# Performance work log

Measured on AMD Instinct MI355X. Metric: run time of the kernel, lower is better.

The kernel has to match this reference:

```python
import jax, jax.numpy as jnp
import numpy as np

HEADS = 8
EPS = 1e-5

def _layer_norm(x, gamma, beta):
    mu = jnp.mean(x, axis=-1, keepdims=True)
    var = jnp.var(x, axis=-1, keepdims=True)
    return (x - mu) * jax.lax.rsqrt(var + EPS) * gamma + beta

def setup_inputs() -> dict:
    key = jax.random.key(0)
    ks = jax.random.split(key, 12)
    B, N, D, H = 4, 2048, 512, 2048
    s = lambda d: 1.0 / np.sqrt(d)
    return {
        "x": jax.random.normal(ks[0], (B, N, D), jnp.float32),
        "w_qkv": jax.random.normal(ks[1], (D, 3 * D), jnp.float32) * s(D),
        "b_qkv": jnp.zeros((3 * D,), jnp.float32),
        "w_proj": jax.random.normal(ks[2], (D, D), jnp.float32) * s(D),
        "b_proj": jnp.zeros((D,), jnp.float32),
        "ln1_g": jnp.ones((D,), jnp.float32),
        "ln1_b": jnp.zeros((D,), jnp.float32),
        "w1": jax.random.normal(ks[3], (D, H), jnp.float32) * s(D),
        "b1": jnp.zeros((H,), jnp.float32),
        "w2": jax.random.normal(ks[4], (H, D), jnp.float32) * s(H),
        "b2": jnp.zeros((D,), jnp.float32),
        "ln2_g": jnp.ones((D,), jnp.float32),
        "ln2_b": jnp.zeros((D,), jnp.float32),
    }

def reference(x, w_qkv, b_qkv, w_proj, b_proj, ln1_g, ln1_b, w1, b1, w2, b2, ln2_g, ln2_b):
    B, N, D = x.shape
    hd = D // HEADS
    scaling = hd ** (-0.5)
    # fused QKV projection: [b, n, 3*D] -> u=3, h heads
    qkv = x @ w_qkv + b_qkv
    qkv = qkv.reshape(B, N, 3, HEADS, hd)            # 'b n (u h e)' with u outermost
    q, k, v = (qkv[:, :, 0], qkv[:, :, 1], qkv[:, :, 2])  # each [b, n, h, e]
    q = q.transpose(0, 2, 1, 3); k = k.transpose(0, 2, 1, 3); v = v.transpose(0, 2, 1, 3)
    sim = jnp.einsum('bhqe,bhke->bhqk', q, k)        # NO pre-softmax scaling
    sim = jax.nn.softmax(sim, axis=-1) * scaling     # scaling applied AFTER softmax
    att = jnp.einsum('bhqk,bhke->bhqe', sim, v)
    att = att.transpose(0, 2, 1, 3).reshape(B, N, D)
    att = att @ w_proj + b_proj
    x = _layer_norm(x + att, ln1_g, ln1_b)
    # MLP sublayer (exact GELU as in torch nn.GELU default)
    h = jax.nn.gelu(x @ w1 + b1, approximate=False) @ w2 + b2
    x = _layer_norm(x + h, ln2_g, ln2_b)
    return x
```

## Files before the change

### kernel.cpp

```cpp
#include <hip/hip_runtime.h>

#define HEADS 8
#define Bq 4
#define Nq 2048
#define Dq 512
#define Hq 2048

typedef __bf16 bf16;
typedef __bf16 bf16x8 __attribute__((ext_vector_type(8)));
typedef __bf16 bf16x4 __attribute__((ext_vector_type(4)));
typedef short short4v __attribute__((ext_vector_type(4)));
typedef float f32x4 __attribute__((ext_vector_type(4)));

__device__ __forceinline__ void gload16(const bf16* g, bf16* s) {
  __builtin_amdgcn_global_load_lds(
      (const __attribute__((address_space(1))) void*)g,
      (__attribute__((address_space(3))) void*)s, 16, 0, 0);
}

__device__ __forceinline__ float fexp2(float x) {
#if __has_builtin(__builtin_amdgcn_exp2f)
  return __builtin_amdgcn_exp2f(x);
#else
  return exp2f(x);
#endif
}

__device__ __forceinline__ float frcp(float x) {
#if __has_builtin(__builtin_amdgcn_rcpf)
  return __builtin_amdgcn_rcpf(x);
#else
  return 1.f / x;
#endif
}

__device__ __forceinline__ float fgelu(float v) {
  float u = 0.7978845608f * (v + 0.044715f * v * v * v);
  float e = fexp2(u * 2.885390082f);
  return v * e * frcp(e + 1.f);
}

#define VM_BARRIER(N)                                         \
  do {                                                        \
    asm volatile("s_waitcnt vmcnt(" #N ")" ::: "memory");     \
    __builtin_amdgcn_s_barrier();                             \
    asm volatile("" ::: "memory");                            \
  } while (0)
#define END_BARRIER()                                         \
  do {                                                        \
    asm volatile("" ::: "memory");                            \
    __builtin_amdgcn_s_barrier();                             \
    asm volatile("" ::: "memory");                            \
  } while (0)

__global__ __launch_bounds__(256) void k_cvt_bf16(const float* __restrict__ in,
                                                  bf16* __restrict__ out, int n) {
  int i = (blockIdx.x * 256 + threadIdx.x) * 4;
  if (i >= n) return;
  float4 v = *(const float4*)(in + i);
  union { bf16 h[4]; ushort4 u; } r;
  r.h[0] = (bf16)v.x; r.h[1] = (bf16)v.y; r.h[2] = (bf16)v.z; r.h[3] = (bf16)v.w;
  *(ushort4*)(out + i) = r.u;
}

__global__ __launch_bounds__(256) void k_wtrans(const float* __restrict__ w_qkv,
                                                const float* __restrict__ w_proj,
                                                const float* __restrict__ w1,
                                                const float* __restrict__ w2,
                                                bf16* __restrict__ wqkvT,
                                                bf16* __restrict__ wprojT,
                                                bf16* __restrict__ w1T,
                                                bf16* __restrict__ w2T) {
  __shared__ float t[32][33];
  const int bid = blockIdx.x;
  const float* src;
  bf16* dst;
  int K, N, n0, k0;
  if (bid < 768) {
    src = w_qkv; dst = wqkvT; K = 512; N = 1536;
    n0 = (bid % 48) * 32; k0 = (bid / 48) * 32;
  } else if (bid < 1024) {
    int i = bid - 768;
    src = w_proj; dst = wprojT; K = 512; N = 512;
    n0 = (i % 16) * 32; k0 = (i / 16) * 32;
  } else if (bid < 2048) {
    int i = bid - 1024;
    src = w1; dst = w1T; K = 512; N = 2048;
    n0 = (i % 64) * 32; k0 = (i / 64) * 32;
  } else {
    int i = bid - 2048;
    src = w2; dst = w2T; K = 2048; N = 512;
    n0 = (i % 16) * 32; k0 = (i / 16) * 32;
  }
  const int tx = threadIdx.x, ty = threadIdx.y;
#pragma unroll
  for (int j = 0; j < 32; j += 8)
    t[ty + j][tx] = src[(size_t)(k0 + ty + j) * N + n0 + tx];
  __syncthreads();
#pragma unroll
  for (int j = 0; j < 32; j += 8)
    dst[(size_t)(n0 + ty + j) * K + k0 + tx] = (bf16)t[tx][ty + j];
}

template <int BM, bool GELU, bool RESID, bool STORE_BF16>
__global__ __launch_bounds__(512, 4) void k_gemm(const bf16* __restrict__ A,
                                                 const bf16* __restrict__ BT,
                                                 const float* __restrict__ bias,
                                                 const float* __restrict__ resid,
                                                 void* __restrict__ Cout,
                                                 int M, int N, int K, int GX) {
  constexpr int MI = BM / 32;
  constexpr int AROUNDS = BM / 64;
  constexpr size_t MAIN = (size_t)2 * (BM + 128) * 64 * 2;
  constexpr size_t CST = (size_t)BM * 136 * (STORE_BF16 ? 2 : 4);
  constexpr size_t SMEM = MAIN > CST ? MAIN : CST;
  __shared__ __align__(16) char smem[SMEM];
  bf16* Asb = (bf16*)smem;
  bf16* Bsb = Asb + 2 * BM * 64;

  const int nwg = gridDim.x;
  const int id = blockIdx.x;
  const int swz = (id & 7) * (nwg >> 3) + (id >> 3);
  const int bx = swz % GX, by = swz / GX;
  const int m0 = by * BM, n0 = bx * 128;

  const int tid = threadIdx.x, lane = tid & 63, wid = tid >> 6;
  const int wr = wid >> 2, wc = wid & 3;
  const int r16 = lane & 15, g = lane >> 4;
  const int lrow = lane >> 3;
  const int sch = (lane & 7) ^ lrow;

  f32x4 acc[MI][2] = {};

  const int NT = K >> 6;
  auto stage = [&](int t, int buf) {
    const int k0 = t << 6;
#pragma unroll
    for (int i = 0; i < AROUNDS; i++) {
      int row = i * 64 + wid * 8 + lrow;
      gload16(A + (size_t)(m0 + row) * K + k0 + sch * 8,
              Asb + buf * BM * 64 + (i * 64 + wid * 8) * 64);
    }
#pragma unroll
    for (int i = 0; i < 2; i++) {
      int row = i * 64 + wid * 8 + lrow;
      gload16(BT + (size_t)(n0 + row) * K + k0 + sch * 8,
              Bsb + buf * 128 * 64 + (i * 64 + wid * 8) * 64);
    }
  };
  auto compute = [&](const bf16* Ab, const bf16* Bb) {
#pragma unroll
    for (int kk = 0; kk < 2; kk++) {
      bf16x8 af[MI], bfr[2];
#pragma unroll
      for (int mi = 0; mi < MI; mi++)
        af[mi] = *(const bf16x8*)(Ab + (wr * (BM / 2) + mi * 16 + r16) * 64 +
                                  (((kk * 4 + g) ^ (r16 & 7)) * 8));
#pragma unroll
      for (int ni = 0; ni < 2; ni++)
        bfr[ni] = *(const bf16x8*)(Bb + (wc * 32 + ni * 16 + r16) * 64 +
                                   (((kk * 4 + g) ^ (r16 & 7)) * 8));
#pragma unroll
      for (int mi = 0; mi < MI; mi++)
#pragma unroll
        for (int ni = 0; ni < 2; ni++)
          acc[mi][ni] = __builtin_amdgcn_mfma_f32_16x16x32_bf16(af[mi], bfr[ni],
                                                                acc[mi][ni], 0, 0, 0);
    }
  };

  stage(0, 0);
  __syncthreads();

  for (int t = 0; t < NT; t += 2) {
    if (t + 1 < NT) stage(t + 1, 1);
    compute(Asb, Bsb);
    __syncthreads();
    if (t + 2 < NT) stage(t + 2, 0);
    compute(Asb + BM * 64, Bsb + 128 * 64);
    __syncthreads();
  }

  float bv[2];
#pragma unroll
  for (int ni = 0; ni < 2; ni++) bv[ni] = bias[n0 + wc * 32 + ni * 16 + r16];

  if (STORE_BF16) {
    bf16* Cl = (bf16*)smem;
#pragma unroll
    for (int mi = 0; mi < MI; mi++)
#pragma unroll
      for (int ni = 0; ni < 2; ni++)
#pragma unroll
        for (int r = 0; r < 4; r++) {
          float v = acc[mi][ni][r] + bv[ni];
          if (GELU) v = fgelu(v);
          Cl[(wr * (BM / 2) + mi * 16 + 4 * g + r) * 136 + wc * 32 + ni * 16 + r16] =
              (bf16)v;
        }
    __syncthreads();
    constexpr int ROWS_PER = 512 * 8 / 128;
#pragma unroll
    for (int rr = 0; rr < BM / ROWS_PER; rr++) {
      int row = rr * ROWS_PER + (tid >> 4);
      int cc = (tid & 15) * 8;
      bf16x8 v = *(const bf16x8*)(Cl + row * 136 + cc);
      *(bf16x8*)((bf16*)Cout + (size_t)(m0 + row) * N + n0 + cc) = v;
    }
  } else {
    float* Cl = (float*)smem;
#pragma unroll
    for (int mi = 0; mi < MI; mi++)
#pragma unroll
      for (int ni = 0; ni < 2; ni++)
#pragma unroll
        for (int r = 0; r < 4; r++) {
          float v = acc[mi][ni][r] + bv[ni];
          if (GELU) v = fgelu(v);
          Cl[(wr * (BM / 2) + mi * 16 + 4 * g + r) * 136 + wc * 32 + ni * 16 + r16] = v;
        }
    __syncthreads();
    constexpr int ROWS_PER = 512 * 4 / 128;
#pragma unroll
    for (int rr = 0; rr < BM / ROWS_PER; rr++) {
      int row = rr * ROWS_PER + (tid >> 5);
      int cc = (tid & 31) * 4;
      f32x4 v = *(const f32x4*)(Cl + row * 136 + cc);
      if (RESID) {
        f32x4 rv = *(const f32x4*)(resid + (size_t)(m0 + row) * N + n0 + cc);
        v += rv;
      }
      *(f32x4*)((float*)Cout + (size_t)(m0 + row) * N + n0 + cc) = v;
    }
  }
}

__global__ __launch_bounds__(256) void k_vtrans(const bf16* __restrict__ qkv,
                                                bf16* __restrict__ vt) {
  __shared__ bf16 T[64 * 66];
  const int kvb = blockIdx.x, bh = blockIdx.y;
  const int b = bh >> 3, h = bh & 7;
  const int tid = threadIdx.x, lane = tid & 63, w = tid >> 6;
  const bf16* src = qkv + ((size_t)b * Nq + kvb * 64) * (3 * Dq) + 2 * Dq + h * 64;
#pragma unroll
  for (int i = 0; i < 2; i++) {
    int u = tid + i * 256;
    int r = u >> 3, ch = u & 7;
    *(int4*)(&T[r * 66 + ch * 8]) = *(const int4*)(src + (size_t)r * (3 * Dq) + ch * 8);
  }
  __syncthreads();
  bf16* dst = vt + (size_t)bh * 64 * Nq + kvb * 64 + lane;
#pragma unroll
  for (int it = 0; it < 16; it++) {
    int e = w * 16 + it;
    dst[(size_t)e * Nq] = T[lane * 66 + e];
  }
}

__global__ __launch_bounds__(256) void k_attn(const bf16* __restrict__ qkv,
                                              const bf16* __restrict__ vt,
                                              bf16* __restrict__ att) {
  __shared__ bf16 Ks[2][64 * 64];
  __shared__ bf16 Vs[2][64 * 64];
  const int qt = blockIdx.y, b = blockIdx.x >> 3, h = blockIdx.x & 7;
  const int tid = threadIdx.x, lane = tid & 63, wid = tid >> 6;
  const int r16 = lane & 15, g = lane >> 4;
  const size_t base = (size_t)b * Nq * (3 * Dq);
  const bf16* qp = qkv + base + h * 64;
  const bf16* kp = qkv + base + Dq + h * 64;
  const bf16* vtp = vt + (size_t)(b * HEADS + h) * 64 * Nq;
  const int q0 = qt * 64 + wid * 16;

  bf16x8 qf[2];
#pragma unroll
  for (int kk = 0; kk < 2; kk++) {
    bf16x8 q = *(const bf16x8*)(qp + (size_t)(q0 + r16) * (3 * Dq) + kk * 32 + g * 8);
#pragma unroll
    for (int j = 0; j < 8; j++) q[j] = (bf16)((float)q[j] * 1.44269504f);
    qf[kk] = q;
  }

  const int srow = lane >> 3;
  const int sch = (lane & 7) ^ srow;
  int fsrc[2];
#pragma unroll
  for (int i = 0; i < 2; i++) {
    int d = (wid * 2 + i) * 8 + srow;
    fsrc[i] = ((d >> 5) << 5) + 8 * ((d & 15) >> 2) + 4 * ((d >> 4) & 1) + (d & 3);
  }

  bf16x8 ones8;
#pragma unroll
  for (int j = 0; j < 8; j++) ones8[j] = (bf16)1.f;

  f32x4 o[4] = {};
  f32x4 ol = {};

#pragma unroll
  for (int i = 0; i < 2; i++) {
    int br = (wid * 2 + i) * 8;
    gload16(kp + (size_t)fsrc[i] * (3 * Dq) + sch * 8, &Ks[0][br * 64]);
    gload16(vtp + (size_t)(br + srow) * Nq + sch * 8, &Vs[0][br * 64]);
  }
  __syncthreads();

  const int NTILES = Nq / 64;
  auto tile = [&](int t, int c) {
    if (t + 1 < NTILES) {
      const int kv1 = (t + 1) * 64;
#pragma unroll
      for (int i = 0; i < 2; i++) {
        int br = (wid * 2 + i) * 8;
        gload16(kp + (size_t)(kv1 + fsrc[i]) * (3 * Dq) + sch * 8,
                &Ks[c ^ 1][br * 64]);
        gload16(vtp + (size_t)(br + srow) * Nq + kv1 + sch * 8, &Vs[c ^ 1][br * 64]);
      }
      VM_BARRIER(4);
    } else {
      VM_BARRIER(0);
    }

    f32x4 s[4] = {};
    __builtin_amdgcn_s_setprio(1);
#pragma unroll
    for (int kk = 0; kk < 2; kk++)
#pragma unroll
      for (int nt = 0; nt < 4; nt++) {
        const bf16x8 kf = *(const bf16x8*)(
            &Ks[c][(nt * 16 + r16) * 64 + (((4 * kk + g) ^ (r16 & 7)) * 8)]);
        s[nt] = __builtin_amdgcn_mfma_f32_16x16x32_bf16(kf, qf[kk], s[nt], 0, 0, 0);
      }
    __builtin_amdgcn_s_setprio(0);

#pragma unroll
    for (int nt = 0; nt < 4; nt++)
#pragma unroll
      for (int r = 0; r < 4; r++) s[nt][r] = fexp2(s[nt][r]);

    bf16x8 pb[2];
#pragma unroll
    for (int kk = 0; kk < 2; kk++) {
      bf16x8 t8;
#pragma unroll
      for (int r = 0; r < 4; r++) {
        t8[r] = (bf16)s[2 * kk][r];
        t8[4 + r] = (bf16)s[2 * kk + 1][r];
      }
      pb[kk] = t8;
    }

    __builtin_amdgcn_s_setprio(1);
    ol = __builtin_amdgcn_mfma_f32_16x16x32_bf16(ones8, pb[0], ol, 0, 0, 0);
    ol = __builtin_amdgcn_mfma_f32_16x16x32_bf16(ones8, pb[1], ol, 0, 0, 0);
#pragma unroll
    for (int kk = 0; kk < 2; kk++)
#pragma unroll
      for (int ot = 0; ot < 4; ot++) {
        const bf16x8 vf = *(const bf16x8*)(
            &Vs[c][(ot * 16 + r16) * 64 + (((kk * 4 + g) ^ (r16 & 7)) * 8)]);
        o[ot] = __builtin_amdgcn_mfma_f32_16x16x32_bf16(vf, pb[kk], o[ot], 0, 0, 0);
      }
    __builtin_amdgcn_s_setprio(0);
    END_BARRIER();
  };

  for (int t = 0; t < NTILES; t += 2) {
    tile(t, 0);
    tile(t + 1, 1);
  }

  asm volatile("s_nop 7\ns_nop 7");

  const float li = 0.125f / ol[0];
  const size_t rowoff = ((size_t)b * Nq + q0 + r16) * Dq + h * 64;
#pragma unroll
  for (int ot = 0; ot < 4; ot++) {
    union { bf16 h[4]; ushort4 u; } r4;
#pragma unroll
    for (int r = 0; r < 4; r++) r4.h[r] = (bf16)(o[ot][r] * li);
    *(ushort4*)(att + rowoff + ot * 16 + 4 * g) = r4.u;
  }
}

template <bool WB>
__global__ __launch_bounds__(256) void k_ln(const float* __restrict__ in,
                                            const float* __restrict__ gamma,
                                            const float* __restrict__ beta,
                                            float* __restrict__ outf,
                                            bf16* __restrict__ outb) {
  const int row = blockIdx.x * 4 + threadIdx.y;
  const int lane = threadIdx.x;
  const float* p = in + (size_t)row * Dq + lane * 8;
  float4 a = *(const float4*)p;
  float4 c = *(const float4*)(p + 4);
  float vals[8] = {a.x, a.y, a.z, a.w, c.x, c.y, c.z, c.w};
  float s = 0.f, q = 0.f;
#pragma unroll
  for (int j = 0; j < 8; j++) { s += vals[j]; q += vals[j] * vals[j]; }
#pragma unroll
  for (int off = 1; off < 64; off <<= 1) {
    s += __shfl_xor(s, off);
    q += __shfl_xor(q, off);
  }
  float mean = s * (1.f / Dq);
  float var = q * (1.f / Dq) - mean * mean;
  float rstd = rsqrtf(var + 1e-5f);
  float of[8];
#pragma unroll
  for (int j = 0; j < 8; j++) {
    int col = lane * 8 + j;
    of[j] = (vals[j] - mean) * rstd * gamma[col] + beta[col];
  }
  float4* op = (float4*)(outf + (size_t)row * Dq + lane * 8);
  op[0] = make_float4(of[0], of[1], of[2], of[3]);
  op[1] = make_float4(of[4], of[5], of[6], of[7]);
  if (WB) {
    union { bf16 h[8]; ushort4 u[2]; } rr;
#pragma unroll
    for (int j = 0; j < 8; j++) rr.h[j] = (bf16)of[j];
    ushort4* ob = (ushort4*)(outb + (size_t)row * Dq + lane * 8);
    ob[0] = rr.u[0];
    ob[1] = rr.u[1];
  }
}

extern "C" void kernel_launch(void* const* d_in, const int* in_sizes, int n_in,
                              void* d_out, int out_size, void* d_ws, size_t ws_size,
                              hipStream_t stream) {
  const float* x      = (const float*)d_in[0];
  const float* w_qkv  = (const float*)d_in[1];
  const float* b_qkv  = (const float*)d_in[2];
  const float* w_proj = (const float*)d_in[3];
  const float* b_proj = (const float*)d_in[4];
  const float* ln1_g  = (const float*)d_in[5];
  const float* ln1_b  = (const float*)d_in[6];
  const float* w1     = (const float*)d_in[7];
  const float* b1     = (const float*)d_in[8];
  const float* w2     = (const float*)d_in[9];
  const float* b2     = (const float*)d_in[10];
  const float* ln2_g  = (const float*)d_in[11];
  const float* ln2_b  = (const float*)d_in[12];
  float* out = (float*)d_out;

  const int M = Bq * Nq;

  char* p = (char*)d_ws;
  auto alloc = [&](size_t bytes) -> void* {
    char* r = p;
    p += (bytes + 255) & ~(size_t)255;
    return (void*)r;
  };
  bf16* xb     = (bf16*)alloc((size_t)M * Dq * 2);
  bf16* qkvb   = (bf16*)alloc((size_t)M * 3 * Dq * 2);
  bf16* wqkvT  = (bf16*)alloc((size_t)3 * Dq * Dq * 2);
  bf16* wprojT = (bf16*)alloc((size_t)Dq * Dq * 2);
  bf16* w1T    = (bf16*)alloc((size_t)Hq * Dq * 2);
  bf16* w2T    = (bf16*)alloc((size_t)Dq * Hq * 2);
  float* y1    = (float*)alloc((size_t)M * Dq * 4);
  float* x1f   = (float*)alloc((size_t)M * Dq * 4);
  bf16* x1b    = (bf16*)alloc((size_t)M * Dq * 2);
  bf16* hb     = (bf16*)alloc((size_t)M * Hq * 2);
  bf16* attb   = xb;
  bf16* vtb    = hb;

  dim3 tb(32, 8);
  k_cvt_bf16<<<(M * Dq / 4 + 255) / 256, 256, 0, stream>>>(x, xb, M * Dq);
  k_wtrans<<<3072, tb, 0, stream>>>(w_qkv, w_proj, w1, w2, wqkvT, wprojT, w1T, w2T);

  k_gemm<128, false, false, true><<<768, 512, 0, stream>>>(
      xb, wqkvT, b_qkv, nullptr, qkvb, M, 3 * Dq, Dq, 12);
  k_vtrans<<<dim3(Nq / 64, Bq * HEADS), 256, 0, stream>>>(qkvb, vtb);
  k_attn<<<dim3(Bq * HEADS, Nq / 64), 256, 0, stream>>>(qkvb, vtb, attb);
  k_gemm<64, false, true, false><<<512, 512, 0, stream>>>(
      attb, wprojT, b_proj, x, y1, M, Dq, Dq, 4);
  k_ln<true><<<M / 4, dim3(64, 4), 0, stream>>>(y1, ln1_g, ln1_b, x1f, x1b);
  k_gemm<128, true, false, true><<<1024, 512, 0, stream>>>(
      x1b, w1T, b1, nullptr, hb, M, Hq, Dq, 16);
  k_gemm<64, false, true, false><<<512, 512, 0, stream>>>(
      hb, w2T, b2, x1f, y1, M, Dq, Hq, 4);
  k_ln<false><<<M / 4, dim3(64, 4), 0, stream>>>(y1, ln2_g, ln2_b, out, nullptr);
}
```

Baseline: 161.4 us.

## Fuse V transpose into QKV GEMM epilogue and store residual sums in bf16

```diff
diff --git a/kernel.cpp b/kernel.cpp
--- a/kernel.cpp
+++ b/kernel.cpp
@@ -102,17 +102,18 @@
     dst[(size_t)(n0 + ty + j) * K + k0 + tx] = (bf16)t[tx][ty + j];
 }
 
-template <int BM, bool GELU, bool RESID, bool STORE_BF16>
+template <int BM, bool GELU, bool RESID, bool STORE_BF16, bool VTOUT = false>
 __global__ __launch_bounds__(512, 4) void k_gemm(const bf16* __restrict__ A,
                                                  const bf16* __restrict__ BT,
                                                  const float* __restrict__ bias,
                                                  const float* __restrict__ resid,
                                                  void* __restrict__ Cout,
+                                                 bf16* __restrict__ vt,
                                                  int M, int N, int K, int GX) {
   constexpr int MI = BM / 32;
   constexpr int AROUNDS = BM / 64;
   constexpr size_t MAIN = (size_t)2 * (BM + 128) * 64 * 2;
-  constexpr size_t CST = (size_t)BM * 136 * (STORE_BF16 ? 2 : 4);
+  constexpr size_t CST = (size_t)BM * 136 * ((STORE_BF16 && !RESID) ? 2 : 4);
   constexpr size_t SMEM = MAIN > CST ? MAIN : CST;
   __shared__ __align__(16) char smem[SMEM];
   bf16* Asb = (bf16*)smem;
@@ -185,7 +186,31 @@
 #pragma unroll
   for (int ni = 0; ni < 2; ni++) bv[ni] = bias[n0 + wc * 32 + ni * 16 + r16];
 
-  if (STORE_BF16) {
+  if (VTOUT && n0 >= 1024) {
+    bf16* Clt = (bf16*)smem;
+#pragma unroll
+    for (int mi = 0; mi < MI; mi++)
+#pragma unroll
+      for (int ni = 0; ni < 2; ni++)
+#pragma unroll
+        for (int r = 0; r < 4; r++) {
+          float v = acc[mi][ni][r] + bv[ni];
+          Clt[(wc * 32 + ni * 16 + r16) * 136 + (wr * 64 + mi * 16 + 4 * g + r)] =
+              (bf16)v;
+        }
+    __syncthreads();
+    const int c = tid >> 2, q = tid & 3;
+    const int j = (n0 - 1024) >> 7;
+    const int h = 2 * j + (c >> 6), e = c & 63;
+    const int bb = m0 >> 11, nb = m0 & 2047;
+    bf16* dst = vt + ((size_t)(bb * 8 + h) * 64 + e) * Nq + nb + q * 32;
+#pragma unroll
+    for (int i = 0; i < 4; i++)
+      *(int4*)(dst + i * 8) = *(const int4*)(&Clt[c * 136 + q * 32 + i * 8]);
+    return;
+  }
+
+  if (STORE_BF16 && !RESID) {
     bf16* Cl = (bf16*)smem;
 #pragma unroll
     for (int mi = 0; mi < MI; mi++)
@@ -206,6 +231,32 @@
       int cc = (tid & 15) * 8;
       bf16x8 v = *(const bf16x8*)(Cl + row * 136 + cc);
       *(bf16x8*)((bf16*)Cout + (size_t)(m0 + row) * N + n0 + cc) = v;
+    }
+  } else if (STORE_BF16 && RESID) {
+    float* Clf = (float*)smem;
+#pragma unroll
+    for (int mi = 0; mi < MI; mi++)
+#pragma unroll
+      for (int ni = 0; ni < 2; ni++)
+#pragma unroll
+        for (int r = 0; r < 4; r++) {
+          float v = acc[mi][ni][r] + bv[ni];
+          if (GELU) v = fgelu(v);
+          Clf[(wr * (BM / 2) + mi * 16 + 4 * g + r) * 136 + wc * 32 + ni * 16 + r16] = v;
+        }
+    __syncthreads();
+    constexpr int ROWS_PER = 512 * 4 / 128;
+#pragma unroll
+    for (int rr = 0; rr < BM / ROWS_PER; rr++) {
+      int row = rr * ROWS_PER + (tid >> 5);
+      int cc = (tid & 31) * 4;
+      f32x4 v = *(const f32x4*)(Clf + row * 136 + cc);
+      f32x4 rv = *(const f32x4*)(resid + (size_t)(m0 + row) * N + n0 + cc);
+      v += rv;
+      union { bf16 h[4]; uint2 u; } r4;
+#pragma unroll
+      for (int r = 0; r < 4; r++) r4.h[r] = (bf16)v[r];
+      *(uint2*)((bf16*)Cout + (size_t)(m0 + row) * N + n0 + cc) = r4.u;
     }
   } else {
     float* Cl = (float*)smem;
@@ -232,28 +283,6 @@
       }
       *(f32x4*)((float*)Cout + (size_t)(m0 + row) * N + n0 + cc) = v;
     }
-  }
-}
-
-__global__ __launch_bounds__(256) void k_vtrans(const bf16* __restrict__ qkv,
-                                                bf16* __restrict__ vt) {
-  __shared__ bf16 T[64 * 66];
-  const int kvb = blockIdx.x, bh = blockIdx.y;
-  const int b = bh >> 3, h = bh & 7;
-  const int tid = threadIdx.x, lane = tid & 63, w = tid >> 6;
-  const bf16* src = qkv + ((size_t)b * Nq + kvb * 64) * (3 * Dq) + 2 * Dq + h * 64;
-#pragma unroll
-  for (int i = 0; i < 2; i++) {
-    int u = tid + i * 256;
-    int r = u >> 3, ch = u & 7;
-    *(int4*)(&T[r * 66 + ch * 8]) = *(const int4*)(src + (size_t)r * (3 * Dq) + ch * 8);
-  }
-  __syncthreads();
-  bf16* dst = vt + (size_t)bh * 64 * Nq + kvb * 64 + lane;
-#pragma unroll
-  for (int it = 0; it < 16; it++) {
-    int e = w * 16 + it;
-    dst[(size_t)e * Nq] = T[lane * 66 + e];
   }
 }
 
@@ -383,17 +412,18 @@
 }
 
 template <bool WB>
-__global__ __launch_bounds__(256) void k_ln(const float* __restrict__ in,
+__global__ __launch_bounds__(256) void k_ln(const bf16* __restrict__ in,
                                             const float* __restrict__ gamma,
                                             const float* __restrict__ beta,
                                             float* __restrict__ outf,
                                             bf16* __restrict__ outb) {
   const int row = blockIdx.x * 4 + threadIdx.y;
   const int lane = threadIdx.x;
-  const float* p = in + (size_t)row * Dq + lane * 8;
-  float4 a = *(const float4*)p;
-  float4 c = *(const float4*)(p + 4);
-  float vals[8] = {a.x, a.y, a.z, a.w, c.x, c.y, c.z, c.w};
+  const bf16* p = in + (size_t)row * Dq + lane * 8;
+  bf16x8 a = *(const bf16x8*)p;
+  float vals[8];
+#pragma unroll
+  for (int j = 0; j < 8; j++) vals[j] = (float)a[j];
   float s = 0.f, q = 0.f;
 #pragma unroll
   for (int j = 0; j < 8; j++) { s += vals[j]; q += vals[j] * vals[j]; }
@@ -456,7 +486,7 @@
   bf16* wprojT = (bf16*)alloc((size_t)Dq * Dq * 2);
   bf16* w1T    = (bf16*)alloc((size_t)Hq * Dq * 2);
   bf16* w2T    = (bf16*)alloc((size_t)Dq * Hq * 2);
-  float* y1    = (float*)alloc((size_t)M * Dq * 4);
+  bf16* y1b    = (bf16*)alloc((size_t)M * Dq * 2);
   float* x1f   = (float*)alloc((size_t)M * Dq * 4);
   bf16* x1b    = (bf16*)alloc((size_t)M * Dq * 2);
   bf16* hb     = (bf16*)alloc((size_t)M * Hq * 2);
@@ -467,16 +497,15 @@
   k_cvt_bf16<<<(M * Dq / 4 + 255) / 256, 256, 0, stream>>>(x, xb, M * Dq);
   k_wtrans<<<3072, tb, 0, stream>>>(w_qkv, w_proj, w1, w2, wqkvT, wprojT, w1T, w2T);
 
-  k_gemm<128, false, false, true><<<768, 512, 0, stream>>>(
-      xb, wqkvT, b_qkv, nullptr, qkvb, M, 3 * Dq, Dq, 12);
-  k_vtrans<<<dim3(Nq / 64, Bq * HEADS), 256, 0, stream>>>(qkvb, vtb);
+  k_gemm<128, false, false, true, true><<<768, 512, 0, stream>>>(
+      xb, wqkvT, b_qkv, nullptr, qkvb, vtb, M, 3 * Dq, Dq, 12);
   k_attn<<<dim3(Bq * HEADS, Nq / 64), 256, 0, stream>>>(qkvb, vtb, attb);
-  k_gemm<64, false, true, false><<<512, 512, 0, stream>>>(
-      attb, wprojT, b_proj, x, y1, M, Dq, Dq, 4);
-  k_ln<true><<<M / 4, dim3(64, 4), 0, stream>>>(y1, ln1_g, ln1_b, x1f, x1b);
+  k_gemm<64, false, true, true><<<512, 512, 0, stream>>>(
+      attb, wprojT, b_proj, x, y1b, nullptr, M, Dq, Dq, 4);
+  k_ln<true><<<M / 4, dim3(64, 4), 0, stream>>>(y1b, ln1_g, ln1_b, x1f, x1b);
   k_gemm<128, true, false, true><<<1024, 512, 0, stream>>>(
-      x1b, w1T, b1, nullptr, hb, M, Hq, Dq, 16);
-  k_gemm<64, false, true, false><<<512, 512, 0, stream>>>(
-      hb, w2T, b2, x1f, y1, M, Dq, Hq, 4);
-  k_ln<false><<<M / 4, dim3(64, 4), 0, stream>>>(y1, ln2_g, ln2_b, out, nullptr);
-}
+      x1b, w1T, b1, nullptr, hb, nullptr, M, Hq, Dq, 16);
+  k_gemm<64, false, true, true><<<512, 512, 0, stream>>>(
+      hb, w2T, b2, x1f, y1b, nullptr, M, Dq, Hq, 4);
+  k_ln<false><<<M / 4, dim3(64, 4), 0, stream>>>(y1b, ln2_g, ln2_b, out, nullptr);
+}
```

New measurement: 154.5 us. 4.3% less time.
